# Kernel tuning notes

Hardware: AMD Instinct MI355X
Metric: run time of the kernel (lower is better)

## Reference

```python
import jax, jax.numpy as jnp
import numpy as np

KS = 5
SIGMA = 2.0
N_BINS = 50
MOMENTUM = 0.9
HALF_KS = (KS - 1) // 2


def _gaussian_kernel_window(ks=KS, sigma=SIGMA):
    # Replicates scipy.ndimage.gaussian_filter1d(delta, sigma, mode='reflect'),
    # then renormalizes, exactly as FDS._get_kernel_window does.
    half = (ks - 1) // 2
    base = np.zeros(ks, np.float32)
    base[half] = 1.0
    r = int(4.0 * sigma + 0.5)  # scipy default truncate=4.0
    j = np.arange(-r, r + 1)
    w = np.exp(-0.5 * (j / sigma) ** 2)
    w = w / w.sum()
    idx = np.arange(-r, ks + r)
    for _ in range(8):  # repeated 'reflect' (edge-excluding-center style: d c b a | a b c d | d c b a)
        idx = np.where(idx < 0, -idx - 1, idx)
        idx = np.where(idx >= ks, 2 * ks - 1 - idx, idx)
    xp = base[idx]
    out = np.array([float(np.dot(w, xp[i:i + 2 * r + 1])) for i in range(ks)], np.float32)
    return out / out.sum()


def setup_inputs() -> dict:
    key = jax.random.key(0)
    k1, k2, k3, k4 = jax.random.split(key, 4)
    N, D = 262144, 512
    features = jax.random.normal(k1, (N, D), dtype=jnp.float32)
    labels = jax.random.randint(k2, (N,), 0, N_BINS, dtype=jnp.int64)
    running_mean = jax.random.normal(k3, (N_BINS, D), dtype=jnp.float32)
    running_var = jax.random.uniform(k4, (N_BINS, D), dtype=jnp.float32) + 0.5
    num_samples_tracked = jnp.zeros((N_BINS,), dtype=jnp.float32)
    kernel_window = jnp.asarray(_gaussian_kernel_window(), dtype=jnp.float32)
    return {
        "features": features,
        "labels": labels,
        "running_mean": running_mean,
        "running_var": running_var,
        "num_samples_tracked": num_samples_tracked,
        "kernel_window": kernel_window,
    }


def _smooth(x, kernel_window):
    # reflect-pad (torch 'reflect': excludes edge) along bin axis, then cross-correlate (F.conv1d)
    top = x[HALF_KS:0:-1]              # [half_ks, D]
    bot = x[-2:-2 - HALF_KS:-1]        # [half_ks, D]
    xp = jnp.concatenate([top, x, bot], axis=0)  # [B + 2*half_ks, D]
    B = x.shape[0]
    windows = jnp.stack([xp[i:i + B] for i in range(KS)], axis=0)  # [ks, B, D]
    return jnp.einsum("k,kbd->bd", kernel_window, windows)


def reference(features, labels, running_mean, running_var, num_samples_tracked, kernel_window):
    # --- segmented per-bin mean/var (single pass, replaces the Python loop over labels) ---
    N = features.shape[0]
    labels = labels.astype(jnp.int32)
    counts = jax.ops.segment_sum(jnp.ones((N,), features.dtype), labels, num_segments=N_BINS)  # [B]
    sums = jax.ops.segment_sum(features, labels, num_segments=N_BINS)                          # [B, D]
    sumsq = jax.ops.segment_sum(features * features, labels, num_segments=N_BINS)              # [B, D]
    safe_n = jnp.maximum(counts, 1.0)
    mean = sums / safe_n[:, None]
    # unbiased var for n>1; biased (=0) for n==1, matching torch.var unbiased toggle
    var = (sumsq - safe_n[:, None] * mean * mean) / jnp.maximum(counts - 1.0, 1.0)[:, None]

    present = (counts > 0)[:, None]
    f = MOMENTUM
    new_mean = jnp.where(present, (1.0 - f) * mean + f * running_mean, running_mean)
    new_var = jnp.where(present, (1.0 - f) * var + f * running_var, running_var)
    new_num = num_samples_tracked + counts

    # --- update_smoothed_stats: conv1d smoothing over the bin axis ---
    smoothed_mean = _smooth(new_mean, kernel_window)
    smoothed_var = _smooth(new_var, kernel_window)
    return new_mean, new_var, new_num, smoothed_mean, smoothed_var
```

## Files before the change

### kernel.cpp

```cpp
#include <hip/hip_runtime.h>

#define NB 50
#define DD 512
#define KSZ 5
#define SORT_ROWS 4096
#define EPT 16
#define RPW 64
#define UNR 8

typedef float f4 __attribute__((ext_vector_type(4)));

__global__ __launch_bounds__(256) void fds_sort(
    const int* __restrict__ labels,
    int*       __restrict__ packed,
    float*     __restrict__ g_cnt)
{
    __shared__ int s_hist[NB];
    __shared__ int s_cur[NB];
    const int tid  = threadIdx.x;
    const int base = blockIdx.x * SORT_ROWS;

    if (tid < NB) s_hist[tid] = 0;
    __syncthreads();

    int lab[EPT];
#pragma unroll
    for (int j = 0; j < EPT; ++j) {
        lab[j] = labels[base + j * 256 + tid];
        __hip_atomic_fetch_add(&s_hist[lab[j]], 1,
                               __ATOMIC_RELAXED, __HIP_MEMORY_SCOPE_WORKGROUP);
    }
    __syncthreads();

    if (tid == 0) {
        int run = 0;
        for (int b = 0; b < NB; ++b) { s_cur[b] = run; run += s_hist[b]; }
    }
    __syncthreads();

    if (tid < NB)
        __hip_atomic_fetch_add(&g_cnt[tid], (float)s_hist[tid],
                               __ATOMIC_RELAXED, __HIP_MEMORY_SCOPE_AGENT);

#pragma unroll
    for (int j = 0; j < EPT; ++j) {
        const int l   = lab[j];
        const int pos = __hip_atomic_fetch_add(&s_cur[l], 1,
                              __ATOMIC_RELAXED, __HIP_MEMORY_SCOPE_WORKGROUP);
        const int row = base + j * 256 + tid;
        packed[base + pos] = (row << 6) | l;
    }
}

__device__ __forceinline__ void flush4(
    float* __restrict__ g_sum, float* __restrict__ g_sq,
    int cur, int c0, f4 sum, f4 sq)
{
    float* ps = &g_sum[cur * DD + c0];
    float* pq = &g_sq [cur * DD + c0];
#pragma unroll
    for (int c = 0; c < 4; ++c) {
        __hip_atomic_fetch_add(ps + c, sum[c],
                               __ATOMIC_RELAXED, __HIP_MEMORY_SCOPE_AGENT);
        __hip_atomic_fetch_add(pq + c, sq[c],
                               __ATOMIC_RELAXED, __HIP_MEMORY_SCOPE_AGENT);
    }
}

__global__ __launch_bounds__(256) void fds_reduce(
    const float* __restrict__ features,
    const int*   __restrict__ packed,
    float* __restrict__ g_sum,
    float* __restrict__ g_sq)
{
    const int tid  = threadIdx.x;
    const int wave = tid >> 6;
    const int lane = tid & 63;
    const int gw   = blockIdx.x * 4 + wave;
    const int cg2    = gw & 1;
    const int rchunk = gw >> 1;
    const int r0  = rchunk * RPW;
    const int c0  = cg2 * 256 + lane * 4;
    const f4* __restrict__ f4p = (const f4*)features;

    f4 sum = (f4)0.f, sq = (f4)0.f;
    int cur = packed[r0] & 63;

    int pk[UNR];
#pragma unroll
    for (int j = 0; j < UNR; ++j) pk[j] = packed[r0 + j];

    for (int it = 0; it < RPW; it += UNR) {
        f4 v[UNR];
#pragma unroll
        for (int j = 0; j < UNR; ++j)
            v[j] = __builtin_nontemporal_load(
                f4p + (size_t)(pk[j] >> 6) * (DD / 4) + cg2 * 64 + lane);

        int pk2[UNR];
        const int nb = (it + UNR < RPW) ? (r0 + it + UNR) : r0;
#pragma unroll
        for (int j = 0; j < UNR; ++j) pk2[j] = packed[nb + j];

#pragma unroll
        for (int j = 0; j < UNR; ++j) {
            const int l = pk[j] & 63;
            if (l != cur) {
                flush4(g_sum, g_sq, cur, c0, sum, sq);
                sum = (f4)0.f; sq = (f4)0.f; cur = l;
            }
            sum += v[j];
            sq  += v[j] * v[j];
        }
#pragma unroll
        for (int j = 0; j < UNR; ++j) pk[j] = pk2[j];
    }
    flush4(g_sum, g_sq, cur, c0, sum, sq);
}

__global__ __launch_bounds__(256) void fds_finalize(
    const float* __restrict__ g_sum, const float* __restrict__ g_sq,
    const float* __restrict__ g_cnt,
    const float* __restrict__ running_mean, const float* __restrict__ running_var,
    const float* __restrict__ num_tracked, const float* __restrict__ kwin,
    float* __restrict__ out)
{
    __shared__ float s_cnt[NB];
    __shared__ float s_w[KSZ];
    const int tid = threadIdx.x;
    if (tid < NB)  s_cnt[tid] = g_cnt[tid];
    if (tid < KSZ) s_w[tid]   = kwin[tid];
    __syncthreads();

    const int idx = blockIdx.x * 256 + tid;
    const int b = idx / DD;
    const int d = idx - b * DD;

    float sm = 0.f, sv = 0.f, my_nm = 0.f, my_nv = 0.f;
#pragma unroll
    for (int k = 0; k < KSZ; ++k) {
        const int i = b + k;
        const int bb = (i < 2) ? (2 - i) : ((i >= NB + 2) ? (2 * NB - i) : (i - 2));
        const float cnt    = s_cnt[bb];
        const float safe_n = fmaxf(cnt, 1.f);
        const float s   = g_sum[bb * DD + d];
        const float sqv = g_sq [bb * DD + d];
        const float mean = s / safe_n;
        const float var  = (sqv - safe_n * mean * mean) / fmaxf(cnt - 1.f, 1.f);
        const float rm = running_mean[bb * DD + d];
        const float rv = running_var [bb * DD + d];
        float nm, nv;
        if (cnt > 0.f) {
            nm = 0.1f * mean + 0.9f * rm;
            nv = 0.1f * var  + 0.9f * rv;
        } else {
            nm = rm; nv = rv;
        }
        sm += s_w[k] * nm;
        sv += s_w[k] * nv;
        if (k == 2) { my_nm = nm; my_nv = nv; }
    }
    out[idx]                    = my_nm;
    out[NB * DD + idx]          = my_nv;
    out[2 * NB * DD + NB + idx] = sm;
    out[3 * NB * DD + NB + idx] = sv;
    if (idx < NB)
        out[2 * NB * DD + idx] = num_tracked[idx] + s_cnt[idx];
}

extern "C" void kernel_launch(void* const* d_in, const int* in_sizes, int n_in,
                              void* d_out, int out_size, void* d_ws, size_t ws_size,
                              hipStream_t stream)
{
    const float* features     = (const float*)d_in[0];
    const int*   labels       = (const int*)  d_in[1];
    const float* running_mean = (const float*)d_in[2];
    const float* running_var  = (const float*)d_in[3];
    const float* num_tracked  = (const float*)d_in[4];
    const float* kwin         = (const float*)d_in[5];
    float* out = (float*)d_out;

    const int N = in_sizes[1];

    float* g_sum  = (float*)d_ws;
    float* g_sq   = g_sum + NB * DD;
    float* g_cnt  = g_sq  + NB * DD;
    int*   packed = (int*)(g_cnt + NB);

    hipMemsetAsync(d_ws, 0, (size_t)(2 * NB * DD + NB) * sizeof(float), stream);

    fds_sort<<<N / SORT_ROWS, 256, 0, stream>>>(labels, packed, g_cnt);

    fds_reduce<<<(N / RPW) * 2 / 4, 256, 0, stream>>>(features, packed, g_sum, g_sq);

    fds_finalize<<<NB * DD / 256, 256, 0, stream>>>(
        g_sum, g_sq, g_cnt, running_mean, running_var, num_tracked, kwin, out);
}
```

Measured before the change: 709.4 us.

## Replace global atomic flushes with per-block-bin partial sums and a reduction kernel

The reduce kernel now assigns one wave pair to each (sort block, bin) segment using per-block bin offsets recorded by the sort kernel. Each segment writes its sum and sum-of-squares to a partials buffer instead of issuing float atomics to global memory. A new partsum kernel then reduces the 64 partials per bin. This removes atomic contention and divergent flushes, but segments are unevenly sized (around 82 rows each), it adds a kernel launch, and it writes about 13 MB of partials to global memory.

Measured after the change: 692.6 us. 1.02x faster.

```diff
diff --git a/kernel.cpp b/kernel.cpp
--- a/kernel.cpp
+++ b/kernel.cpp
@@ -5,7 +5,6 @@
 #define KSZ 5
 #define SORT_ROWS 4096
 #define EPT 16
-#define RPW 64
 #define UNR 8
 
 typedef float f4 __attribute__((ext_vector_type(4)));
@@ -13,6 +12,7 @@
 __global__ __launch_bounds__(256) void fds_sort(
     const int* __restrict__ labels,
     int*       __restrict__ packed,
+    int*       __restrict__ bofs,
     float*     __restrict__ g_cnt)
 {
     __shared__ int s_hist[NB];
@@ -38,9 +38,13 @@
     }
     __syncthreads();
 
-    if (tid < NB)
+    if (tid < NB) {
         __hip_atomic_fetch_add(&g_cnt[tid], (float)s_hist[tid],
                                __ATOMIC_RELAXED, __HIP_MEMORY_SCOPE_AGENT);
+        bofs[blockIdx.x * (NB + 1) + tid] = s_cur[tid];
+    }
+    if (tid == 0) bofs[blockIdx.x * (NB + 1) + NB] = SORT_ROWS;
+    __syncthreads();
 
 #pragma unroll
     for (int j = 0; j < EPT; ++j) {
@@ -52,70 +56,65 @@
     }
 }
 
-__device__ __forceinline__ void flush4(
-    float* __restrict__ g_sum, float* __restrict__ g_sq,
-    int cur, int c0, f4 sum, f4 sq)
-{
-    float* ps = &g_sum[cur * DD + c0];
-    float* pq = &g_sq [cur * DD + c0];
-#pragma unroll
-    for (int c = 0; c < 4; ++c) {
-        __hip_atomic_fetch_add(ps + c, sum[c],
-                               __ATOMIC_RELAXED, __HIP_MEMORY_SCOPE_AGENT);
-        __hip_atomic_fetch_add(pq + c, sq[c],
-                               __ATOMIC_RELAXED, __HIP_MEMORY_SCOPE_AGENT);
-    }
-}
-
 __global__ __launch_bounds__(256) void fds_reduce(
     const float* __restrict__ features,
     const int*   __restrict__ packed,
-    float* __restrict__ g_sum,
-    float* __restrict__ g_sq)
+    const int*   __restrict__ bofs,
+    float*       __restrict__ part,
+    int nseg)
 {
     const int tid  = threadIdx.x;
     const int wave = tid >> 6;
     const int lane = tid & 63;
     const int gw   = blockIdx.x * 4 + wave;
-    const int cg2    = gw & 1;
-    const int rchunk = gw >> 1;
-    const int r0  = rchunk * RPW;
-    const int c0  = cg2 * 256 + lane * 4;
-    const f4* __restrict__ f4p = (const f4*)features;
+    const int half = gw & 1;
+    const int seg  = gw >> 1;
+    const int blk  = seg / NB;
+    const int bin  = seg - blk * NB;
+    const int base = blk * SORT_ROWS;
+    const int s    = bofs[blk * (NB + 1) + bin];
+    const int e    = bofs[blk * (NB + 1) + bin + 1];
+    const int c    = half * 64 + lane;
+    const f4* __restrict__ fp = (const f4*)features;
 
     f4 sum = (f4)0.f, sq = (f4)0.f;
-    int cur = packed[r0] & 63;
-
-    int pk[UNR];
-#pragma unroll
-    for (int j = 0; j < UNR; ++j) pk[j] = packed[r0 + j];
-
-    for (int it = 0; it < RPW; it += UNR) {
+    for (int i0 = s; i0 < e; i0 += UNR) {
+        const int n = e - i0;
+        int pk[UNR];
+#pragma unroll
+        for (int j = 0; j < UNR; ++j)
+            pk[j] = packed[base + i0 + (j < n ? j : 0)];
         f4 v[UNR];
 #pragma unroll
         for (int j = 0; j < UNR; ++j)
             v[j] = __builtin_nontemporal_load(
-                f4p + (size_t)(pk[j] >> 6) * (DD / 4) + cg2 * 64 + lane);
-
-        int pk2[UNR];
-        const int nb = (it + UNR < RPW) ? (r0 + it + UNR) : r0;
-#pragma unroll
-        for (int j = 0; j < UNR; ++j) pk2[j] = packed[nb + j];
-
-#pragma unroll
-        for (int j = 0; j < UNR; ++j) {
-            const int l = pk[j] & 63;
-            if (l != cur) {
-                flush4(g_sum, g_sq, cur, c0, sum, sq);
-                sum = (f4)0.f; sq = (f4)0.f; cur = l;
-            }
-            sum += v[j];
-            sq  += v[j] * v[j];
-        }
-#pragma unroll
-        for (int j = 0; j < UNR; ++j) pk[j] = pk2[j];
-    }
-    flush4(g_sum, g_sq, cur, c0, sum, sq);
+                fp + (size_t)(pk[j] >> 6) * (DD / 4) + c);
+#pragma unroll
+        for (int j = 0; j < UNR; ++j)
+            if (j < n) { sum += v[j]; sq += v[j] * v[j]; }
+    }
+
+    f4* ps = (f4*)part;
+    ps[(size_t)seg * (DD / 4) + c]          = sum;
+    ps[(size_t)(nseg + seg) * (DD / 4) + c] = sq;
+}
+
+__global__ __launch_bounds__(256) void fds_partsum(
+    const float* __restrict__ part, int nblk,
+    float* __restrict__ g_sum, float* __restrict__ g_sq)
+{
+    const int idx = blockIdx.x * 256 + threadIdx.x;
+    const int bin = idx / DD;
+    const int d   = idx - bin * DD;
+    const int nseg = nblk * NB;
+    float s = 0.f, q = 0.f;
+#pragma unroll 4
+    for (int blk = 0; blk < nblk; ++blk) {
+        s += part[(size_t)(blk * NB + bin) * DD + d];
+        q += part[(size_t)(nseg + blk * NB + bin) * DD + d];
+    }
+    g_sum[idx] = s;
+    g_sq [idx] = q;
 }
 
 __global__ __launch_bounds__(256) void fds_finalize(
@@ -180,18 +179,26 @@
     const float* kwin         = (const float*)d_in[5];
     float* out = (float*)d_out;
 
-    const int N = in_sizes[1];
+    const int N    = in_sizes[1];
+    const int nblk = N / SORT_ROWS;
+    const int nseg = nblk * NB;
 
     float* g_sum  = (float*)d_ws;
     float* g_sq   = g_sum + NB * DD;
     float* g_cnt  = g_sq  + NB * DD;
     int*   packed = (int*)(g_cnt + NB);
-
-    hipMemsetAsync(d_ws, 0, (size_t)(2 * NB * DD + NB) * sizeof(float), stream);
-
-    fds_sort<<<N / SORT_ROWS, 256, 0, stream>>>(labels, packed, g_cnt);
-
-    fds_reduce<<<(N / RPW) * 2 / 4, 256, 0, stream>>>(features, packed, g_sum, g_sq);
+    int*   bofs   = packed + N;
+    size_t off    = ((size_t)((char*)(bofs + nblk * (NB + 1)) - (char*)d_ws) + 15)
+                    & ~(size_t)15;
+    float* part   = (float*)((char*)d_ws + off);
+
+    hipMemsetAsync(g_cnt, 0, NB * sizeof(float), stream);
+
+    fds_sort<<<nblk, 256, 0, stream>>>(labels, packed, bofs, g_cnt);
+
+    fds_reduce<<<nseg * 2 / 4, 256, 0, stream>>>(features, packed, bofs, part, nseg);
+
+    fds_partsum<<<NB * DD / 256, 256, 0, stream>>>(part, nblk, g_sum, g_sq);
 
     fds_finalize<<<NB * DD / 256, 256, 0, stream>>>(
         g_sum, g_sq, g_cnt, running_mean, running_var, num_tracked, kwin, out);
```
